# Optimization experiments

Hardware: AMD Instinct MI355X
Metric: run time of the kernel (lower is better)

## Reference

```python
import jax, jax.numpy as jnp
import numpy as np
import math

B, NI, NU, D, H, MAXNB, T = 1024, 50000, 20000, 256, 4, 20, 1000


def _cosine_sqrt_ab():
    t = jnp.linspace(0.0, T, T + 1) / T
    ab = jnp.cos((t + 0.008) / 1.008 * math.pi / 2) ** 2
    ab = ab / ab[0]
    ab = ab[1:]
    return jnp.sqrt(ab), jnp.sqrt(1.0 - ab)


def _ln(x, g, b, eps=1e-5):
    m = jnp.mean(x, -1, keepdims=True)
    v = jnp.var(x, -1, keepdims=True)
    return (x - m) / jnp.sqrt(v + eps) * g + b


def _mha(q, k, v, wqkv, bqkv, wo, bo):
    # torch nn.MultiheadAttention (batch_first) with packed in_proj
    d = q.shape[-1]
    dh = d // H
    wq, wk, wv = jnp.split(wqkv, 3, axis=0)
    bq, bk, bv = jnp.split(bqkv, 3, axis=0)
    def heads(x, w, bb):
        y = x @ w.T + bb
        return y.reshape(x.shape[0], x.shape[1], H, dh).transpose(0, 2, 1, 3)
    qh, kh, vh = heads(q, wq, bq), heads(k, wk, bk), heads(v, wv, bv)
    att = jax.nn.softmax(jnp.einsum('bhqd,bhkd->bhqk', qh, kh) / math.sqrt(dh), axis=-1)
    o = jnp.einsum('bhqk,bhkd->bhqd', att, vh)
    o = o.transpose(0, 2, 1, 3).reshape(q.shape[0], q.shape[1], d)
    return o @ wo.T + bo


def setup_inputs() -> dict:
    key = jax.random.key(0)
    ks = iter(jax.random.split(key, 64))
    p = lambda shape, s=0.02: jax.random.normal(next(ks), shape, jnp.float32) * s
    inp = {}
    inp['x0'] = (jax.random.uniform(next(ks), (B, NI)) < 0.05).astype(jnp.float32)
    inp['user_ids'] = jax.random.randint(next(ks), (B,), 0, NU)
    inp['t'] = jax.random.randint(next(ks), (B,), 0, T)
    inp['noise'] = jax.random.normal(next(ks), (B, D), jnp.float32)
    inp['neighbor_idx'] = jax.random.randint(next(ks), (NU, MAXNB), 0, NI)
    inp['item_emb'] = p((NI, D), 0.01)
    inp['enc_w1'] = p((2 * D, NI), 0.01); inp['enc_b1'] = jnp.zeros((2 * D,))
    inp['enc_w2'] = p((D, 2 * D)); inp['enc_b2'] = jnp.zeros((D,))
    inp['dec_w1'] = p((2 * D, D)); inp['dec_b1'] = jnp.zeros((2 * D,))
    inp['dec_w2'] = p((NI, 2 * D)); inp['dec_b2'] = jnp.zeros((NI,))
    inp['up_w'] = p((D, D)); inp['up_b'] = jnp.zeros((D,))
    inp['ip_w'] = p((D, D)); inp['ip_b'] = jnp.zeros((D,))
    inp['te_w1'] = p((32, 1)); inp['te_b1'] = jnp.zeros((32,))
    inp['te_w2'] = p((D, 32)); inp['te_b2'] = jnp.zeros((D,))
    inp['ca_wqkv'] = p((3 * D, D)); inp['ca_bqkv'] = jnp.zeros((3 * D,))
    inp['ca_wo'] = p((D, D)); inp['ca_bo'] = jnp.zeros((D,))
    inp['sa_wqkv'] = p((3 * D, D)); inp['sa_bqkv'] = jnp.zeros((3 * D,))
    inp['sa_wo'] = p((D, D)); inp['sa_bo'] = jnp.zeros((D,))
    inp['n1_g'] = jnp.ones((D,)); inp['n1_b'] = jnp.zeros((D,))
    inp['n2_g'] = jnp.ones((D,)); inp['n2_b'] = jnp.zeros((D,))
    inp['ff_w1'] = p((2 * D, D)); inp['ff_b1'] = jnp.zeros((2 * D,))
    inp['ff_w2'] = p((D, 2 * D)); inp['ff_b2'] = jnp.zeros((D,))
    return inp


def reference(x0, user_ids, t, noise, neighbor_idx, item_emb,
              enc_w1, enc_b1, enc_w2, enc_b2, dec_w1, dec_b1, dec_w2, dec_b2,
              up_w, up_b, ip_w, ip_b, te_w1, te_b1, te_w2, te_b2,
              ca_wqkv, ca_bqkv, ca_wo, ca_bo, sa_wqkv, sa_bqkv, sa_wo, sa_bo,
              n1_g, n1_b, n2_g, n2_b, ff_w1, ff_b1, ff_w2, ff_b2):
    gelu = lambda x: jax.nn.gelu(x, approximate=False)
    # encoder: (B, NI) -> (B, D)
    z0 = gelu(x0 @ enc_w1.T + enc_b1) @ enc_w2.T + enc_b2
    sqrt_ab, sqrt_1ab = _cosine_sqrt_ab()
    z_t = sqrt_ab[t][:, None] * z0 + sqrt_1ab[t][:, None] * noise
    # vectorized padded neighbor gather: (B, MAXNB, D)
    nb = item_emb[neighbor_idx[user_ids]]
    t_norm = t.astype(jnp.float32) / T
    # denoiser
    q = (z_t @ up_w.T + up_b)[:, None, :]
    kv = nb @ ip_w.T + ip_b
    te = jax.nn.silu(t_norm[:, None] @ te_w1.T + te_b1) @ te_w2.T + te_b2
    q = q + te[:, None, :]
    ca = _mha(q, kv, kv, ca_wqkv, ca_bqkv, ca_wo, ca_bo)
    h = _ln(q + ca, n1_g, n1_b)[:, 0, :]
    sa = _mha(h[:, None], h[:, None], h[:, None], sa_wqkv, sa_bqkv, sa_wo, sa_bo)[:, 0, :]
    h = _ln(h + sa, n2_g, n2_b)
    z_pred = h + (gelu(h @ ff_w1.T + ff_b1) @ ff_w2.T + ff_b2)
    diff_loss = jnp.mean((z_pred - z0) ** 2)
    logits = gelu(z0 @ dec_w1.T + dec_b1) @ dec_w2.T + dec_b2
    recon = jnp.mean(jax.nn.softplus(logits) - logits * x0)
    return diff_loss + 0.1 * recon
```

## Files before the change

kernel.cpp:

```cpp
#include <hip/hip_runtime.h>
#include <math.h>

#define NI   50000
#define Tt   1000
#define KP   50176
#define MW   1568
#define NPAD 50048

typedef __bf16 bf16x8 __attribute__((ext_vector_type(8)));
typedef float  f32x4  __attribute__((ext_vector_type(4)));

__device__ __forceinline__ unsigned short f2bf(float f) {
  unsigned u = __float_as_uint(f);
  u += 0x7FFFu + ((u >> 16) & 1u);
  return (unsigned short)(u >> 16);
}
__device__ __forceinline__ float bf2f(unsigned short u) {
  return __uint_as_float(((unsigned)u) << 16);
}
__device__ __forceinline__ unsigned pack2(float a, float b) {
  return (unsigned)f2bf(a) | ((unsigned)f2bf(b) << 16);
}
__device__ __forceinline__ f32x4 mfma16(const unsigned short* a, const unsigned short* b, f32x4 c) {
  typedef unsigned short u16x8 __attribute__((ext_vector_type(8)));
  u16x8 av = *(const u16x8*)a;
  u16x8 bv = *(const u16x8*)b;
  return __builtin_amdgcn_mfma_f32_16x16x32_bf16(
      __builtin_bit_cast(bf16x8, av), __builtin_bit_cast(bf16x8, bv), c, 0, 0, 0);
}
__device__ __forceinline__ float gelu_f(float x) {
  return 0.5f * x * (1.f + erff(x * 0.70710678118654752f));
}

#define GLD16(gsrc, ldst) __builtin_amdgcn_global_load_lds( \
    (const __attribute__((address_space(1))) unsigned int*)(const void*)(gsrc), \
    (__attribute__((address_space(3))) unsigned int*)(void*)(ldst), 16, 0, 0)

__global__ __launch_bounds__(256) void bm_expand(
    const float* __restrict__ x0, unsigned int* __restrict__ xmask,
    unsigned short* __restrict__ x0b)
{
  __shared__ unsigned int nib[256];
  int r = blockIdx.y, tid = threadIdx.x;
  int c0 = blockIdx.x * 2048;
  int k = c0 + tid * 8;
  const float* row = x0 + (size_t)r * NI;
  float4 a = make_float4(0.f, 0.f, 0.f, 0.f), b = a;
  if (k + 8 <= NI) {
    a = *(const float4*)(row + k);
    b = *(const float4*)(row + k + 4);
  }
  uint4 o;
  o.x = (a.x != 0.f ? 0x3F80u : 0u) | (a.y != 0.f ? 0x3F800000u : 0u);
  o.y = (a.z != 0.f ? 0x3F80u : 0u) | (a.w != 0.f ? 0x3F800000u : 0u);
  o.z = (b.x != 0.f ? 0x3F80u : 0u) | (b.y != 0.f ? 0x3F800000u : 0u);
  o.w = (b.z != 0.f ? 0x3F80u : 0u) | (b.w != 0.f ? 0x3F800000u : 0u);
  if (k < KP) *(uint4*)(x0b + (size_t)r * KP + k) = o;
  unsigned bits8 =
      (a.x != 0.f ? 1u : 0u)  | (a.y != 0.f ? 2u : 0u)  |
      (a.z != 0.f ? 4u : 0u)  | (a.w != 0.f ? 8u : 0u)  |
      (b.x != 0.f ? 16u : 0u) | (b.y != 0.f ? 32u : 0u) |
      (b.z != 0.f ? 64u : 0u) | (b.w != 0.f ? 128u : 0u);
  nib[tid] = bits8;
  __syncthreads();
  if (tid < 64) {
    unsigned wv = nib[tid * 4] | (nib[tid * 4 + 1] << 8) |
                  (nib[tid * 4 + 2] << 16) | (nib[tid * 4 + 3] << 24);
    int widx = (c0 >> 5) + tid;
    if (widx < MW) xmask[(size_t)r * MW + widx] = wv;
  }
}

__global__ __launch_bounds__(256) void cvt_w1(const float* __restrict__ src,
                                              unsigned short* __restrict__ dst) {
  int c = blockIdx.x * 2048 + threadIdx.x * 8;
  if (c >= KP) return;
  int r = blockIdx.y;
  const float* s = src + (size_t)r * NI;
  uint4 o;
  if (c + 8 <= NI) {
    float4 a = *(const float4*)(s + c), b = *(const float4*)(s + c + 4);
    o.x = pack2(a.x, a.y); o.y = pack2(a.z, a.w);
    o.z = pack2(b.x, b.y); o.w = pack2(b.z, b.w);
  } else {
    float v[8];
#pragma unroll
    for (int i = 0; i < 8; ++i) v[i] = (c + i < NI) ? s[c + i] : 0.f;
    o.x = pack2(v[0], v[1]); o.y = pack2(v[2], v[3]);
    o.z = pack2(v[4], v[5]); o.w = pack2(v[6], v[7]);
  }
  *(uint4*)(dst + (size_t)r * KP + c) = o;
}

__global__ __launch_bounds__(256) void cvt_w2n(const float* __restrict__ src,
                                               unsigned short* __restrict__ dst) {
  size_t idx = ((size_t)blockIdx.x * 256 + threadIdx.x) * 8;
  float4 a = *(const float4*)(src + idx), b = *(const float4*)(src + idx + 4);
  uint4 o;
  o.x = pack2(a.x, a.y); o.y = pack2(a.z, a.w);
  o.z = pack2(b.x, b.y); o.w = pack2(b.z, b.w);
  *(uint4*)(dst + idx) = o;
}

__global__ __launch_bounds__(256) void cvt_many(
    const float* s0, const float* s1, const float* s2, const float* s3,
    const float* s4, const float* s5, const float* s6,
    unsigned short* d0, unsigned short* d1, unsigned short* d2, unsigned short* d3,
    unsigned short* d4, unsigned short* d5, unsigned short* d6)
{
  const float* srcs[7] = {s0, s1, s2, s3, s4, s5, s6};
  unsigned short* dsts[7] = {d0, d1, d2, d3, d4, d5, d6};
  const int ns[7] = {131072, 65536, 65536, 65536, 131072, 131072, 131072};
  int j = blockIdx.y;
  int i = (blockIdx.x * 256 + threadIdx.x) * 8;
  if (i >= ns[j]) return;
  float4 a = *(const float4*)(srcs[j] + i), b = *(const float4*)(srcs[j] + i + 4);
  uint4 o;
  o.x = pack2(a.x, a.y); o.y = pack2(a.z, a.w);
  o.z = pack2(b.x, b.y); o.w = pack2(b.z, b.w);
  *(uint4*)(dsts[j] + i) = o;
}

__global__ __launch_bounds__(256) void compose_k(
    const float* __restrict__ ca_wqkv, const float* __restrict__ ca_bqkv,
    const float* __restrict__ ip_w, const float* __restrict__ ip_b,
    const float* __restrict__ sa_wqkv, const float* __restrict__ sa_bqkv,
    const float* __restrict__ sa_wo, const float* __restrict__ sa_bo,
    unsigned short* __restrict__ Wkv, float* __restrict__ bkv,
    unsigned short* __restrict__ Wsa, float* __restrict__ bsa)
{
  int b = blockIdx.x, k = threadIdx.x;
  if (b < 512) {
    const float* wrow = ca_wqkv + (size_t)(256 + b) * 256;
    float s = 0.f;
    for (int c = 0; c < 256; ++c) s += wrow[c] * ip_w[c * 256 + k];
    Wkv[b * 256 + k] = f2bf(s);
    if (k == 0) {
      float sb = 0.f;
      for (int c = 0; c < 256; ++c) sb += wrow[c] * ip_b[c];
      bkv[b] = sb + ca_bqkv[256 + b];
    }
  } else {
    int i = b - 512;
    const float* worow = sa_wo + (size_t)i * 256;
    float s = 0.f;
    for (int c = 0; c < 256; ++c) s += worow[c] * sa_wqkv[(512 + c) * 256 + k];
    Wsa[i * 256 + k] = f2bf(s);
    if (k == 0) {
      float sb = 0.f;
      for (int c = 0; c < 256; ++c) sb += worow[c] * sa_bqkv[512 + c];
      bsa[i] = sb + sa_bo[i];
    }
  }
}

template<int T>
__global__ __launch_bounds__(256) void gemm128(
    const unsigned short* __restrict__ A, int lda,
    const unsigned short* __restrict__ Bw, int ldb,
    const float* __restrict__ bias, void* __restrict__ Cv, int ldc, int K,
    const unsigned int* __restrict__ xmask, float* __restrict__ loss, int Nvalid)
{
  __shared__ __align__(16) unsigned short As[128 * 32];
  __shared__ __align__(16) unsigned short Bs[128 * 32];
  __shared__ unsigned int msk[128][4];
  __shared__ float red[4];
  const int tid = threadIdx.x;
  int m0, n0, kb = 0, kc = 0, iters;
  if (T == 2) {
    int id = blockIdx.x;
    int g = (id & 7) + 8 * (id >> 6);
    m0 = ((id >> 3) & 7) * 128;
    n0 = (g & 3) * 128;
    kc = g >> 2;
    kb = kc * 1568;
    iters = 49;
  } else if (T == 1) {
    int id = blockIdx.x;
    int n = (id & 7) + 8 * (id >> 6);
    if (n >= 391) return;
    m0 = ((id >> 3) & 7) * 128;
    n0 = n * 128;
    iters = 16;
  } else {
    m0 = blockIdx.x * 128; n0 = blockIdx.y * 128;
    iters = K >> 5;
  }
  const int w = tid >> 6, l = tid & 63;
  const int wm = (w >> 1) * 64, wn = (w & 1) * 64;
  const int fr = l & 15, fo = (l >> 4) * 8;
  const int s0 = tid, s1 = tid + 256;
  f32x4 acc[4][4] = {};
  for (int it = 0; it < iters; ++it) {
    int k0 = kb + it * 32;
    __syncthreads();
    GLD16(A  + (size_t)(m0 + (s0 >> 2)) * lda + k0 + (s0 & 3) * 8, &As[s0 * 8]);
    GLD16(A  + (size_t)(m0 + (s1 >> 2)) * lda + k0 + (s1 & 3) * 8, &As[s1 * 8]);
    GLD16(Bw + (size_t)(n0 + (s0 >> 2)) * ldb + k0 + (s0 & 3) * 8, &Bs[s0 * 8]);
    GLD16(Bw + (size_t)(n0 + (s1 >> 2)) * ldb + k0 + (s1 & 3) * 8, &Bs[s1 * 8]);
    __syncthreads();
    const unsigned short *ap[4], *bp[4];
#pragma unroll
    for (int i = 0; i < 4; ++i) {
      ap[i] = &As[(wm + 16 * i + fr) * 32 + fo];
      bp[i] = &Bs[(wn + 16 * i + fr) * 32 + fo];
    }
#pragma unroll
    for (int i = 0; i < 4; ++i)
#pragma unroll
      for (int j = 0; j < 4; ++j)
        acc[i][j] = mfma16(ap[i], bp[j], acc[i][j]);
  }
  const int cr = (l >> 4) * 4, cc = l & 15;
  if (T == 0) {
    unsigned short* Cb = (unsigned short*)Cv;
#pragma unroll
    for (int j = 0; j < 4; ++j) {
      int n = n0 + wn + 16 * j + cc;
      float bv = bias[n];
#pragma unroll
      for (int i = 0; i < 4; ++i)
#pragma unroll
        for (int r = 0; r < 4; ++r) {
          int m = m0 + wm + 16 * i + cr + r;
          Cb[(size_t)m * ldc + n] = f2bf(acc[i][j][r] + bv);
        }
    }
  } else if (T == 2) {
    float* Cp = ((kc < 16) ? (float*)Cv : loss) + (size_t)(kc & 15) * 524288;
#pragma unroll
    for (int i = 0; i < 4; ++i)
#pragma unroll
      for (int j = 0; j < 4; ++j) {
        int n = n0 + wn + 16 * j + cc;
#pragma unroll
        for (int r = 0; r < 4; ++r) {
          int m = m0 + wm + 16 * i + cr + r;
          Cp[(size_t)m * 512 + n] = acc[i][j][r];
        }
      }
  } else {
    {
      int row = tid >> 1, p = tid & 1;
      *(uint2*)&msk[row][p * 2] =
          *(const uint2*)(xmask + (size_t)(m0 + row) * MW + (n0 >> 5) + p * 2);
    }
    __syncthreads();
    float ts = 0.f;
#pragma unroll
    for (int j = 0; j < 4; ++j) {
      int nl = wn + 16 * j + cc;
      int n = n0 + nl;
      if (n < Nvalid) {
        float bv = bias[n];
#pragma unroll
        for (int i = 0; i < 4; ++i)
#pragma unroll
          for (int r = 0; r < 4; ++r) {
            int ml = wm + 16 * i + cr + r;
            float lg = acc[i][j][r] + bv;
            float sp = fmaxf(lg, 0.f) + __logf(1.f + __expf(-fabsf(lg)));
            unsigned word = msk[ml][nl >> 5];
            ts += sp - (((word >> (nl & 31)) & 1u) ? lg : 0.f);
          }
      }
    }
    for (int off = 32; off > 0; off >>= 1) ts += __shfl_xor(ts, off);
    if (l == 0) red[w] = ts;
    __syncthreads();
    if (tid == 0) atomicAdd(loss, red[0] + red[1] + red[2] + red[3]);
  }
}

template<int EPI>
__global__ __launch_bounds__(256) void gemm64(
    const unsigned short* __restrict__ A, int lda,
    const unsigned short* __restrict__ Bw, int ldb,
    const float* __restrict__ bias, void* __restrict__ Cv, int ldc, int K,
    const void* __restrict__ R0, const void* __restrict__ R1, const void* __restrict__ R2,
    void* __restrict__ W0, void* __restrict__ W1, float* __restrict__ loss)
{
  __shared__ __align__(16) unsigned short As[64 * 32];
  __shared__ __align__(16) unsigned short Bs[64 * 32];
  __shared__ float red[4];
  const int tid = threadIdx.x;
  const int m0 = blockIdx.x * 64, n0 = blockIdx.y * 64;
  const int w = tid >> 6, l = tid & 63;
  const int wm = (w >> 1) * 32, wn = (w & 1) * 32;
  const int fr = l & 15, fo = (l >> 4) * 8;
  const int srow = tid >> 2, scol = (tid & 3) * 8;
  f32x4 acc[2][2] = {};
  for (int k0 = 0; k0 < K; k0 += 32) {
    __syncthreads();
    GLD16(A  + (size_t)(m0 + srow) * lda + k0 + scol, &As[tid * 8]);
    GLD16(Bw + (size_t)(n0 + srow) * ldb + k0 + scol, &Bs[tid * 8]);
    __syncthreads();
    const unsigned short* ap0 = &As[(wm +      fr) * 32 + fo];
    const unsigned short* ap1 = &As[(wm + 16 + fr) * 32 + fo];
    const unsigned short* bp0 = &Bs[(wn +      fr) * 32 + fo];
    const unsigned short* bp1 = &Bs[(wn + 16 + fr) * 32 + fo];
    acc[0][0] = mfma16(ap0, bp0, acc[0][0]);
    acc[0][1] = mfma16(ap0, bp1, acc[0][1]);
    acc[1][0] = mfma16(ap1, bp0, acc[1][0]);
    acc[1][1] = mfma16(ap1, bp1, acc[1][1]);
  }
  const int cr = (l >> 4) * 4, cc = l & 15;
  float ts = 0.f;
#pragma unroll
  for (int i = 0; i < 2; ++i)
#pragma unroll
    for (int j = 0; j < 2; ++j) {
      int n = n0 + wn + 16 * j + cc;
      float bv = bias[n];
#pragma unroll
      for (int r = 0; r < 4; ++r) {
        int m = m0 + wm + 16 * i + cr + r;
        float v = acc[i][j][r] + bv;
        size_t idx = (size_t)m * ldc + n;
        if (EPI == 0) ((float*)Cv)[idx] = v;
        if (EPI == 1) ((unsigned short*)Cv)[idx] = f2bf(v);
        if (EPI == 2) ((unsigned short*)Cv)[idx] = f2bf(gelu_f(v));
        if (EPI == 3) {
          ((float*)Cv)[idx] = v;
          ((unsigned short*)W0)[idx] = f2bf(v);
          float zt = ((const float*)R1)[m] * v +
                     ((const float*)R2)[m] * ((const float*)R0)[idx];
          ((unsigned short*)W1)[idx] = f2bf(zt);
        }
        if (EPI == 4) {
          v += ((const float*)R0)[idx];
          ((unsigned short*)Cv)[idx] = f2bf(v);
        }
        if (EPI == 5) {
          v += bf2f(((const unsigned short*)R0)[idx]);
          float d = v - ((const float*)R1)[idx];
          ts += d * d;
        }
      }
    }
  if (EPI == 5) {
    for (int off = 32; off > 0; off >>= 1) ts += __shfl_xor(ts, off);
    if (l == 0) red[w] = ts;
    __syncthreads();
    if (tid == 0) atomicAdd(loss, red[0] + red[1] + red[2] + red[3]);
  }
}

__global__ __launch_bounds__(256) void h1_epi(const float* __restrict__ P0,
                                              const float* __restrict__ P1,
                                              const float* __restrict__ b,
                                              unsigned short* __restrict__ H) {
  int i = blockIdx.x * 256 + threadIdx.x;
  float s = b[i & 511];
#pragma unroll
  for (int k = 0; k < 16; ++k) s += P0[(size_t)k * 524288 + i];
#pragma unroll
  for (int k = 0; k < 16; ++k) s += P1[(size_t)k * 524288 + i];
  H[i] = f2bf(gelu_f(s));
}

__global__ __launch_bounds__(256) void prep_te(
    const int* __restrict__ t,
    const float* __restrict__ te_w1, const float* __restrict__ te_b1,
    const float* __restrict__ te_w2, const float* __restrict__ te_b2,
    float* __restrict__ te, float* __restrict__ sab, float* __restrict__ s1ab)
{
  __shared__ float sj[32];
  int b = blockIdx.x, d = threadIdx.x;
  int ti = t[b];
  float tn = (float)ti / (float)Tt;
  if (d < 32) {
    float a = tn * te_w1[d] + te_b1[d];
    sj[d] = a / (1.f + __expf(-a));
  }
  if (d == 0) {
    double tt = (double)(ti + 1) / (double)Tt;
    double c  = cos((tt + 0.008) / 1.008 * M_PI * 0.5);
    double c0 = cos((0.008) / 1.008 * M_PI * 0.5);
    double ab = (c * c) / (c0 * c0);
    sab[b]  = (float)sqrt(ab);
    s1ab[b] = (float)sqrt(1.0 - ab);
  }
  __syncthreads();
  float accv = te_b2[d];
#pragma unroll
  for (int j = 0; j < 32; ++j) accv += sj[j] * te_w2[d * 32 + j];
  te[(size_t)b * 256 + d] = accv;
}

__global__ __launch_bounds__(256) void gather_nb(
    const int* __restrict__ uid, const int* __restrict__ nidx,
    const float* __restrict__ emb, unsigned short* __restrict__ nb)
{
  int b = blockIdx.x, j = blockIdx.y, d = threadIdx.x;
  int idx = nidx[uid[b] * 20 + j];
  nb[((size_t)b * 20 + j) * 256 + d] = f2bf(emb[(size_t)idx * 256 + d]);
}

__global__ __launch_bounds__(256) void attn_k(
    const float* __restrict__ qh, const unsigned short* __restrict__ kvh,
    unsigned short* __restrict__ o)
{
  int b = blockIdx.x, tid = threadIdx.x;
  int h = tid >> 6, d = tid & 63;
  float qv = qh[(size_t)b * 256 + h * 64 + d];
  const unsigned short* kbase = kvh + (size_t)b * 20 * 512 + h * 64 + d;
  const unsigned short* vbase = kbase + 256;
  float s[20];
#pragma unroll
  for (int k = 0; k < 20; ++k) {
    float p = qv * bf2f(kbase[k * 512]);
    for (int off = 32; off > 0; off >>= 1) p += __shfl_xor(p, off);
    s[k] = p * 0.125f;
  }
  float mx = s[0];
#pragma unroll
  for (int k = 1; k < 20; ++k) mx = fmaxf(mx, s[k]);
  float sum = 0.f;
#pragma unroll
  for (int k = 0; k < 20; ++k) { s[k] = __expf(s[k] - mx); sum += s[k]; }
  float inv = 1.f / sum;
  float ov = 0.f;
#pragma unroll
  for (int k = 0; k < 20; ++k) ov += s[k] * bf2f(vbase[k * 512]);
  o[(size_t)b * 256 + h * 64 + d] = f2bf(ov * inv);
}

__global__ __launch_bounds__(256) void ln_k(
    const unsigned short* __restrict__ X, const unsigned short* __restrict__ Y,
    const float* __restrict__ g, const float* __restrict__ bb,
    unsigned short* __restrict__ out)
{
  __shared__ float rs[4], rs2[4];
  int b = blockIdx.x, d = threadIdx.x;
  size_t i = (size_t)b * 256 + d;
  float v = bf2f(X[i]) + bf2f(Y[i]);
  float s = v, s2 = v * v;
  for (int off = 32; off > 0; off >>= 1) { s += __shfl_xor(s, off); s2 += __shfl_xor(s2, off); }
  int w = d >> 6, l = d & 63;
  if (l == 0) { rs[w] = s; rs2[w] = s2; }
  __syncthreads();
  s  = rs[0] + rs[1] + rs[2] + rs[3];
  s2 = rs2[0] + rs2[1] + rs2[2] + rs2[3];
  float mean = s * (1.f / 256.f);
  float var  = s2 * (1.f / 256.f) - mean * mean;
  out[i] = f2bf((v - mean) * rsqrtf(var + 1e-5f) * g[d] + bb[d]);
}

__global__ void final_k(const float* __restrict__ scal, float* __restrict__ out) {
  out[0] = scal[0] * (1.f / (1024.f * 256.f)) + 0.1f * scal[1] * (1.f / (1024.f * 50000.f));
}

extern "C" void kernel_launch(void* const* d_in, const int* in_sizes, int n_in,
                              void* d_out, int out_size, void* d_ws, size_t ws_size,
                              hipStream_t stream) {
  const float* x0      = (const float*)d_in[0];
  const int*   uid     = (const int*)  d_in[1];
  const int*   t       = (const int*)  d_in[2];
  const float* noise   = (const float*)d_in[3];
  const int*   nidx    = (const int*)  d_in[4];
  const float* item_emb= (const float*)d_in[5];
  const float* enc_w1  = (const float*)d_in[6];
  const float* enc_b1  = (const float*)d_in[7];
  const float* enc_w2  = (const float*)d_in[8];
  const float* enc_b2  = (const float*)d_in[9];
  const float* dec_w1  = (const float*)d_in[10];
  const float* dec_b1  = (const float*)d_in[11];
  const float* dec_w2  = (const float*)d_in[12];
  const float* dec_b2  = (const float*)d_in[13];
  const float* up_w    = (const float*)d_in[14];
  const float* up_b    = (const float*)d_in[15];
  const float* ip_w    = (const float*)d_in[16];
  const float* ip_b    = (const float*)d_in[17];
  const float* te_w1   = (const float*)d_in[18];
  const float* te_b1   = (const float*)d_in[19];
  const float* te_w2   = (const float*)d_in[20];
  const float* te_b2   = (const float*)d_in[21];
  const float* ca_wqkv = (const float*)d_in[22];
  const float* ca_bqkv = (const float*)d_in[23];
  const float* ca_wo   = (const float*)d_in[24];
  const float* ca_bo   = (const float*)d_in[25];
  const float* sa_wqkv = (const float*)d_in[26];
  const float* sa_bqkv = (const float*)d_in[27];
  const float* sa_wo   = (const float*)d_in[28];
  const float* sa_bo   = (const float*)d_in[29];
  const float* n1_g    = (const float*)d_in[30];
  const float* n1_b    = (const float*)d_in[31];
  const float* n2_g    = (const float*)d_in[32];
  const float* n2_b    = (const float*)d_in[33];
  const float* ff_w1   = (const float*)d_in[34];
  const float* ff_b1   = (const float*)d_in[35];
  const float* ff_w2   = (const float*)d_in[36];
  const float* ff_b2   = (const float*)d_in[37];
  (void)in_sizes; (void)n_in; (void)out_size; (void)ws_size;

  float* ws   = (float*)d_ws;
  float* scal = ws;
  float* sab  = ws + 4;
  float* s1ab = sab + 1024;
  float* te   = s1ab + 1024;
  float* qhf  = te + 262144;
  float* z0f  = qhf + 262144;
  float* bkv  = z0f + 262144;
  float* bsa  = bkv + 512;
  unsigned int* xmask = (unsigned int*)(bsa + 256);
  unsigned short* sh  = (unsigned short*)(xmask + 1024 * MW);
  float*          OUTp = (float*)sh;
  unsigned short* nbb  = sh;
  unsigned short* kvhb = nbb + 5242880;
  unsigned short* f1b  = kvhb + 10485760;
  unsigned short* Gb   = f1b + 524288;
  unsigned short* x0b  = Gb + 524288;
  unsigned short* w2n  = x0b;
  unsigned short* w1b  = x0b + (size_t)1024 * KP;
  unsigned short* H1b  = w1b + (size_t)512 * KP;
  unsigned short* z0b  = H1b + 524288;
  unsigned short* ztb  = z0b + 262144;
  unsigned short* qpb  = ztb + 262144;
  unsigned short* ob   = qpb + 262144;
  unsigned short* cab  = ob  + 262144;
  unsigned short* hb   = cab + 262144;
  unsigned short* saob = hb  + 262144;
  unsigned short* h2b  = saob+ 262144;
  unsigned short* enc_w2b = h2b + 262144;
  unsigned short* up_wb   = enc_w2b + 131072;
  unsigned short* ca_wqb  = up_wb + 65536;
  unsigned short* ca_wob  = ca_wqb + 65536;
  unsigned short* ff_w1b  = ca_wob + 65536;
  unsigned short* ff_w2b  = ff_w1b + 131072;
  unsigned short* dec_w1b = ff_w2b + 131072;
  unsigned short* Wkv     = dec_w1b + 131072;
  unsigned short* Wsab    = Wkv + 131072;
  float*          OUTp2   = (float*)(Wsab + 131072);

  hipMemsetAsync(scal, 0, 4 * sizeof(float), stream);

  prep_te<<<1024, 256, 0, stream>>>(t, te_w1, te_b1, te_w2, te_b2, te, sab, s1ab);
  bm_expand<<<dim3(25, 1024), 256, 0, stream>>>(x0, xmask, x0b);
  cvt_w1<<<dim3(25, 512), 256, 0, stream>>>(enc_w1, w1b);
  cvt_many<<<dim3(64, 7), 256, 0, stream>>>(enc_w2, up_w, ca_wqkv, ca_wo, ff_w1, ff_w2, dec_w1,
                                            enc_w2b, up_wb, ca_wqb, ca_wob, ff_w1b, ff_w2b, dec_w1b);
  compose_k<<<768, 256, 0, stream>>>(ca_wqkv, ca_bqkv, ip_w, ip_b,
                                     sa_wqkv, sa_bqkv, sa_wo, sa_bo,
                                     Wkv, bkv, Wsab, bsa);

  gemm128<2><<<1024, 256, 0, stream>>>(
      x0b, KP, w1b, KP, nullptr, OUTp, 512, 1568, nullptr, OUTp2, 0);
  h1_epi<<<2048, 256, 0, stream>>>(OUTp, OUTp2, enc_b1, H1b);

  cvt_w2n<<<12500, 256, 0, stream>>>(dec_w2, w2n);

  gather_nb<<<dim3(1024, 20), 256, 0, stream>>>(uid, nidx, item_emb, nbb);
  gemm128<0><<<dim3(160, 4), 256, 0, stream>>>(
      nbb, 256, Wkv, 256, bkv, kvhb, 512, 256, nullptr, nullptr, 0);

  gemm64<3><<<dim3(16, 4), 256, 0, stream>>>(
      H1b, 512, enc_w2b, 512, enc_b2, z0f, 256, 512, noise, sab, s1ab, z0b, ztb, nullptr);

  gemm64<4><<<dim3(16, 4), 256, 0, stream>>>(
      ztb, 256, up_wb, 256, up_b, qpb, 256, 256, te, nullptr, nullptr, nullptr, nullptr, nullptr);
  gemm64<0><<<dim3(16, 4), 256, 0, stream>>>(
      qpb, 256, ca_wqb, 256, ca_bqkv, qhf, 256, 256,
      nullptr, nullptr, nullptr, nullptr, nullptr, nullptr);

  attn_k<<<1024, 256, 0, stream>>>(qhf, kvhb, ob);
  gemm64<1><<<dim3(16, 4), 256, 0, stream>>>(
      ob, 256, ca_wob, 256, ca_bo, cab, 256, 256,
      nullptr, nullptr, nullptr, nullptr, nullptr, nullptr);
  ln_k<<<1024, 256, 0, stream>>>(qpb, cab, n1_g, n1_b, hb);

  gemm64<1><<<dim3(16, 4), 256, 0, stream>>>(
      hb, 256, Wsab, 256, bsa, saob, 256, 256,
      nullptr, nullptr, nullptr, nullptr, nullptr, nullptr);
  ln_k<<<1024, 256, 0, stream>>>(hb, saob, n2_g, n2_b, h2b);

  gemm64<2><<<dim3(16, 8), 256, 0, stream>>>(
      h2b, 256, ff_w1b, 256, ff_b1, f1b, 512, 256,
      nullptr, nullptr, nullptr, nullptr, nullptr, nullptr);
  gemm64<5><<<dim3(16, 4), 256, 0, stream>>>(
      f1b, 512, ff_w2b, 512, ff_b2, nullptr, 256, 512,
      h2b, z0f, nullptr, nullptr, nullptr, &scal[0]);

  gemm64<2><<<dim3(16, 8), 256, 0, stream>>>(
      z0b, 256, dec_w1b, 256, dec_b1, Gb, 512, 256,
      nullptr, nullptr, nullptr, nullptr, nullptr, nullptr);
  gemm128<1><<<3136, 256, 0, stream>>>(
      Gb, 512, w2n, 512, dec_b2, nullptr, 0, 512, xmask, &scal[1], NI);

  final_k<<<1, 1, 0, stream>>>(scal, (float*)d_out);
}
```

Measured before the change: 919.3 us.

## Double-buffer LDS tiles in gemm128 and gemm64 with explicit waitcnt pipelining

```diff
diff --git a/kernel.cpp b/kernel.cpp
--- a/kernel.cpp
+++ b/kernel.cpp
@@ -35,6 +35,9 @@
 #define GLD16(gsrc, ldst) __builtin_amdgcn_global_load_lds( \
     (const __attribute__((address_space(1))) unsigned int*)(const void*)(gsrc), \
     (__attribute__((address_space(3))) unsigned int*)(void*)(ldst), 16, 0, 0)
+
+#define PIPE_FENCE() __builtin_amdgcn_sched_barrier(0)
+#define RAW_BAR()    __builtin_amdgcn_s_barrier()
 
 __global__ __launch_bounds__(256) void bm_expand(
     const float* __restrict__ x0, unsigned int* __restrict__ xmask,
@@ -161,8 +164,8 @@
     const float* __restrict__ bias, void* __restrict__ Cv, int ldc, int K,
     const unsigned int* __restrict__ xmask, float* __restrict__ loss, int Nvalid)
 {
-  __shared__ __align__(16) unsigned short As[128 * 32];
-  __shared__ __align__(16) unsigned short Bs[128 * 32];
+  __shared__ __align__(16) unsigned short As[2][128 * 32];
+  __shared__ __align__(16) unsigned short Bs[2][128 * 32];
   __shared__ unsigned int msk[128][4];
   __shared__ float red[4];
   const int tid = threadIdx.x;
@@ -190,27 +193,49 @@
   const int wm = (w >> 1) * 64, wn = (w & 1) * 64;
   const int fr = l & 15, fo = (l >> 4) * 8;
   const int s0 = tid, s1 = tid + 256;
+  const unsigned short* Ar0 = A  + (size_t)(m0 + (s0 >> 2)) * lda + (s0 & 3) * 8;
+  const unsigned short* Ar1 = A  + (size_t)(m0 + (s1 >> 2)) * lda + (s1 & 3) * 8;
+  const unsigned short* Br0 = Bw + (size_t)(n0 + (s0 >> 2)) * ldb + (s0 & 3) * 8;
+  const unsigned short* Br1 = Bw + (size_t)(n0 + (s1 >> 2)) * ldb + (s1 & 3) * 8;
   f32x4 acc[4][4] = {};
-  for (int it = 0; it < iters; ++it) {
-    int k0 = kb + it * 32;
-    __syncthreads();
-    GLD16(A  + (size_t)(m0 + (s0 >> 2)) * lda + k0 + (s0 & 3) * 8, &As[s0 * 8]);
-    GLD16(A  + (size_t)(m0 + (s1 >> 2)) * lda + k0 + (s1 & 3) * 8, &As[s1 * 8]);
-    GLD16(Bw + (size_t)(n0 + (s0 >> 2)) * ldb + k0 + (s0 & 3) * 8, &Bs[s0 * 8]);
-    GLD16(Bw + (size_t)(n0 + (s1 >> 2)) * ldb + k0 + (s1 & 3) * 8, &Bs[s1 * 8]);
-    __syncthreads();
-    const unsigned short *ap[4], *bp[4];
-#pragma unroll
-    for (int i = 0; i < 4; ++i) {
-      ap[i] = &As[(wm + 16 * i + fr) * 32 + fo];
-      bp[i] = &Bs[(wn + 16 * i + fr) * 32 + fo];
-    }
-#pragma unroll
-    for (int i = 0; i < 4; ++i)
-#pragma unroll
-      for (int j = 0; j < 4; ++j)
-        acc[i][j] = mfma16(ap[i], bp[j], acc[i][j]);
-  }
+
+#define STG128(IT, BUF) do { int kk_ = kb + (IT) * 32;        \
+    GLD16(Ar0 + kk_, &As[BUF][s0 * 8]);                        \
+    GLD16(Ar1 + kk_, &As[BUF][s1 * 8]);                        \
+    GLD16(Br0 + kk_, &Bs[BUF][s0 * 8]);                        \
+    GLD16(Br1 + kk_, &Bs[BUF][s1 * 8]); } while (0)
+
+#define CMP128(BUF) do {                                       \
+    const unsigned short *ap_[4], *bp_[4];                     \
+    _Pragma("unroll") for (int i_ = 0; i_ < 4; ++i_) {         \
+      ap_[i_] = &As[BUF][(wm + 16 * i_ + fr) * 32 + fo];       \
+      bp_[i_] = &Bs[BUF][(wn + 16 * i_ + fr) * 32 + fo]; }     \
+    _Pragma("unroll") for (int i_ = 0; i_ < 4; ++i_)           \
+    _Pragma("unroll") for (int j_ = 0; j_ < 4; ++j_)           \
+      acc[i_][j_] = mfma16(ap_[i_], bp_[j_], acc[i_][j_]); } while (0)
+
+  STG128(0, 0);
+  STG128(1, 1);
+  for (int it = 0; it < iters; it += 2) {
+    if (it + 1 < iters) asm volatile("s_waitcnt vmcnt(4)" ::: "memory");
+    else                asm volatile("s_waitcnt vmcnt(0)" ::: "memory");
+    PIPE_FENCE(); RAW_BAR(); PIPE_FENCE();
+    CMP128(0);
+    asm volatile("s_waitcnt lgkmcnt(0)" ::: "memory");
+    PIPE_FENCE(); RAW_BAR(); PIPE_FENCE();
+    if (it + 2 < iters) STG128(it + 2, 0);
+    if (it + 1 >= iters) break;
+    if (it + 2 < iters) asm volatile("s_waitcnt vmcnt(4)" ::: "memory");
+    else                asm volatile("s_waitcnt vmcnt(0)" ::: "memory");
+    PIPE_FENCE(); RAW_BAR(); PIPE_FENCE();
+    CMP128(1);
+    asm volatile("s_waitcnt lgkmcnt(0)" ::: "memory");
+    PIPE_FENCE(); RAW_BAR(); PIPE_FENCE();
+    if (it + 3 < iters) STG128(it + 3, 1);
+  }
+#undef STG128
+#undef CMP128
+
   const int cr = (l >> 4) * 4, cc = l & 15;
   if (T == 0) {
     unsigned short* Cb = (unsigned short*)Cv;
@@ -280,8 +305,8 @@
     const void* __restrict__ R0, const void* __restrict__ R1, const void* __restrict__ R2,
     void* __restrict__ W0, void* __restrict__ W1, float* __restrict__ loss)
 {
-  __shared__ __align__(16) unsigned short As[64 * 32];
-  __shared__ __align__(16) unsigned short Bs[64 * 32];
+  __shared__ __align__(16) unsigned short As[2][64 * 32];
+  __shared__ __align__(16) unsigned short Bs[2][64 * 32];
   __shared__ float red[4];
   const int tid = threadIdx.x;
   const int m0 = blockIdx.x * 64, n0 = blockIdx.y * 64;
@@ -289,21 +314,47 @@
   const int wm = (w >> 1) * 32, wn = (w & 1) * 32;
   const int fr = l & 15, fo = (l >> 4) * 8;
   const int srow = tid >> 2, scol = (tid & 3) * 8;
+  const unsigned short* Ar = A  + (size_t)(m0 + srow) * lda + scol;
+  const unsigned short* Br = Bw + (size_t)(n0 + srow) * ldb + scol;
+  const int iters = K >> 5;
   f32x4 acc[2][2] = {};
-  for (int k0 = 0; k0 < K; k0 += 32) {
-    __syncthreads();
-    GLD16(A  + (size_t)(m0 + srow) * lda + k0 + scol, &As[tid * 8]);
-    GLD16(Bw + (size_t)(n0 + srow) * ldb + k0 + scol, &Bs[tid * 8]);
-    __syncthreads();
-    const unsigned short* ap0 = &As[(wm +      fr) * 32 + fo];
-    const unsigned short* ap1 = &As[(wm + 16 + fr) * 32 + fo];
-    const unsigned short* bp0 = &Bs[(wn +      fr) * 32 + fo];
-    const unsigned short* bp1 = &Bs[(wn + 16 + fr) * 32 + fo];
-    acc[0][0] = mfma16(ap0, bp0, acc[0][0]);
-    acc[0][1] = mfma16(ap0, bp1, acc[0][1]);
-    acc[1][0] = mfma16(ap1, bp0, acc[1][0]);
-    acc[1][1] = mfma16(ap1, bp1, acc[1][1]);
-  }
+
+#define STG64(IT, BUF) do { int kk_ = (IT) * 32;               \
+    GLD16(Ar + kk_, &As[BUF][tid * 8]);                        \
+    GLD16(Br + kk_, &Bs[BUF][tid * 8]); } while (0)
+
+#define CMP64(BUF) do {                                        \
+    const unsigned short* a0_ = &As[BUF][(wm +      fr) * 32 + fo]; \
+    const unsigned short* a1_ = &As[BUF][(wm + 16 + fr) * 32 + fo]; \
+    const unsigned short* b0_ = &Bs[BUF][(wn +      fr) * 32 + fo]; \
+    const unsigned short* b1_ = &Bs[BUF][(wn + 16 + fr) * 32 + fo]; \
+    acc[0][0] = mfma16(a0_, b0_, acc[0][0]);                   \
+    acc[0][1] = mfma16(a0_, b1_, acc[0][1]);                   \
+    acc[1][0] = mfma16(a1_, b0_, acc[1][0]);                   \
+    acc[1][1] = mfma16(a1_, b1_, acc[1][1]); } while (0)
+
+  STG64(0, 0);
+  STG64(1, 1);
+  for (int it = 0; it < iters; it += 2) {
+    if (it + 1 < iters) asm volatile("s_waitcnt vmcnt(2)" ::: "memory");
+    else                asm volatile("s_waitcnt vmcnt(0)" ::: "memory");
+    PIPE_FENCE(); RAW_BAR(); PIPE_FENCE();
+    CMP64(0);
+    asm volatile("s_waitcnt lgkmcnt(0)" ::: "memory");
+    PIPE_FENCE(); RAW_BAR(); PIPE_FENCE();
+    if (it + 2 < iters) STG64(it + 2, 0);
+    if (it + 1 >= iters) break;
+    if (it + 2 < iters) asm volatile("s_waitcnt vmcnt(2)" ::: "memory");
+    else                asm volatile("s_waitcnt vmcnt(0)" ::: "memory");
+    PIPE_FENCE(); RAW_BAR(); PIPE_FENCE();
+    CMP64(1);
+    asm volatile("s_waitcnt lgkmcnt(0)" ::: "memory");
+    PIPE_FENCE(); RAW_BAR(); PIPE_FENCE();
+    if (it + 3 < iters) STG64(it + 3, 1);
+  }
+#undef STG64
+#undef CMP64
+
   const int cr = (l >> 4) * 4, cc = l & 15;
   float ts = 0.f;
 #pragma unroll
```

Result: no change. 911.0 us (-0.9%).

## Expand bitmask into bf16 A tiles inside encoder GEMM with double-buffered B

Applied to the files above, without the earlier changes.

```diff
diff --git a/kernel.cpp b/kernel.cpp
--- a/kernel.cpp
+++ b/kernel.cpp
@@ -36,9 +36,11 @@
     (const __attribute__((address_space(1))) unsigned int*)(const void*)(gsrc), \
     (__attribute__((address_space(3))) unsigned int*)(void*)(ldst), 16, 0, 0)
 
+#define PIPE_FENCE() __builtin_amdgcn_sched_barrier(0)
+#define RAW_BAR()    __builtin_amdgcn_s_barrier()
+
 __global__ __launch_bounds__(256) void bm_expand(
-    const float* __restrict__ x0, unsigned int* __restrict__ xmask,
-    unsigned short* __restrict__ x0b)
+    const float* __restrict__ x0, unsigned int* __restrict__ xmask)
 {
   __shared__ unsigned int nib[256];
   int r = blockIdx.y, tid = threadIdx.x;
@@ -50,12 +52,6 @@
     a = *(const float4*)(row + k);
     b = *(const float4*)(row + k + 4);
   }
-  uint4 o;
-  o.x = (a.x != 0.f ? 0x3F80u : 0u) | (a.y != 0.f ? 0x3F800000u : 0u);
-  o.y = (a.z != 0.f ? 0x3F80u : 0u) | (a.w != 0.f ? 0x3F800000u : 0u);
-  o.z = (b.x != 0.f ? 0x3F80u : 0u) | (b.y != 0.f ? 0x3F800000u : 0u);
-  o.w = (b.z != 0.f ? 0x3F80u : 0u) | (b.w != 0.f ? 0x3F800000u : 0u);
-  if (k < KP) *(uint4*)(x0b + (size_t)r * KP + k) = o;
   unsigned bits8 =
       (a.x != 0.f ? 1u : 0u)  | (a.y != 0.f ? 2u : 0u)  |
       (a.z != 0.f ? 4u : 0u)  | (a.w != 0.f ? 8u : 0u)  |
@@ -154,6 +150,97 @@
   }
 }
 
+__global__ __launch_bounds__(256) void enc_gemm(
+    const unsigned int* __restrict__ xmask,
+    const unsigned short* __restrict__ Bw,
+    float* __restrict__ P0, float* __restrict__ P1)
+{
+  __shared__ __align__(16) unsigned short As[128 * 32];
+  __shared__ __align__(16) unsigned short Bs[2][128 * 32];
+  const int tid = threadIdx.x;
+  const int id = blockIdx.x;
+  const int g = (id & 7) + 8 * (id >> 6);
+  const int m0 = ((id >> 3) & 7) * 128;
+  const int n0 = (g & 3) * 128;
+  const int kc = g >> 2;
+  const int kb = kc * 1568;
+  const int w = tid >> 6, l = tid & 63;
+  const int wm = (w >> 1) * 64, wn = (w & 1) * 64;
+  const int fr = l & 15, fo = (l >> 4) * 8;
+  const int s0 = tid, s1 = tid + 256;
+  const unsigned short* Br0 = Bw + (size_t)(n0 + (s0 >> 2)) * KP + kb + (s0 & 3) * 8;
+  const unsigned short* Br1 = Bw + (size_t)(n0 + (s1 >> 2)) * KP + kb + (s1 & 3) * 8;
+  const int arow = tid >> 1, ahalf = tid & 1;
+  const unsigned int* mrowp = xmask + (size_t)(m0 + arow) * MW + (kb >> 5);
+  f32x4 acc[4][4] = {};
+
+#define EXPANDA(VW) do {                                                     \
+    unsigned bits_ = ((VW) >> (ahalf * 16)) & 0xFFFFu;                       \
+    uint4 q0_, q1_;                                                          \
+    q0_.x = (bits_ & 1u     ? 0x3F80u : 0u) | (bits_ & 2u     ? 0x3F800000u : 0u); \
+    q0_.y = (bits_ & 4u     ? 0x3F80u : 0u) | (bits_ & 8u     ? 0x3F800000u : 0u); \
+    q0_.z = (bits_ & 16u    ? 0x3F80u : 0u) | (bits_ & 32u    ? 0x3F800000u : 0u); \
+    q0_.w = (bits_ & 64u    ? 0x3F80u : 0u) | (bits_ & 128u   ? 0x3F800000u : 0u); \
+    q1_.x = (bits_ & 256u   ? 0x3F80u : 0u) | (bits_ & 512u   ? 0x3F800000u : 0u); \
+    q1_.y = (bits_ & 1024u  ? 0x3F80u : 0u) | (bits_ & 2048u  ? 0x3F800000u : 0u); \
+    q1_.z = (bits_ & 4096u  ? 0x3F80u : 0u) | (bits_ & 8192u  ? 0x3F800000u : 0u); \
+    q1_.w = (bits_ & 16384u ? 0x3F80u : 0u) | (bits_ & 32768u ? 0x3F800000u : 0u); \
+    *(uint4*)&As[arow * 32 + ahalf * 16]     = q0_;                          \
+    *(uint4*)&As[arow * 32 + ahalf * 16 + 8] = q1_;                          \
+  } while (0)
+
+#define CMPE(BUF) do {                                                       \
+    const unsigned short *ap_[4], *bp_[4];                                   \
+    _Pragma("unroll") for (int i_ = 0; i_ < 4; ++i_) {                       \
+      ap_[i_] = &As[(wm + 16 * i_ + fr) * 32 + fo];                          \
+      bp_[i_] = &Bs[BUF][(wn + 16 * i_ + fr) * 32 + fo]; }                   \
+    _Pragma("unroll") for (int i_ = 0; i_ < 4; ++i_)                         \
+    _Pragma("unroll") for (int j_ = 0; j_ < 4; ++j_)                         \
+      acc[i_][j_] = mfma16(ap_[i_], bp_[j_], acc[i_][j_]); } while (0)
+
+  {
+    unsigned vm = mrowp[0];
+    GLD16(Br0,      &Bs[0][s0 * 8]);
+    GLD16(Br1,      &Bs[0][s1 * 8]);
+    GLD16(Br0 + 32, &Bs[1][s0 * 8]);
+    GLD16(Br1 + 32, &Bs[1][s1 * 8]);
+    EXPANDA(vm);
+    asm volatile("s_waitcnt vmcnt(2) lgkmcnt(0)" ::: "memory");
+    PIPE_FENCE(); RAW_BAR(); PIPE_FENCE();
+  }
+  for (int it = 0; it < 49; ++it) {
+    unsigned vnext = 0;
+    if (it < 48) vnext = mrowp[it + 1];
+    CMPE(it & 1);
+    if (it == 48) break;
+    PIPE_FENCE(); RAW_BAR(); PIPE_FENCE();
+    if (it < 47) {
+      GLD16(Br0 + (it + 2) * 32, &Bs[it & 1][s0 * 8]);
+      GLD16(Br1 + (it + 2) * 32, &Bs[it & 1][s1 * 8]);
+    }
+    EXPANDA(vnext);
+    if (it < 47) asm volatile("s_waitcnt vmcnt(2) lgkmcnt(0)" ::: "memory");
+    else         asm volatile("s_waitcnt vmcnt(0) lgkmcnt(0)" ::: "memory");
+    PIPE_FENCE(); RAW_BAR(); PIPE_FENCE();
+  }
+#undef EXPANDA
+#undef CMPE
+
+  const int cr = (l >> 4) * 4, cc = l & 15;
+  float* Cp = ((kc < 16) ? P0 : P1) + (size_t)(kc & 15) * 524288;
+#pragma unroll
+  for (int i = 0; i < 4; ++i)
+#pragma unroll
+    for (int j = 0; j < 4; ++j) {
+      int n = n0 + wn + 16 * j + cc;
+#pragma unroll
+      for (int r = 0; r < 4; ++r) {
+        int m = m0 + wm + 16 * i + cr + r;
+        Cp[(size_t)m * 512 + n] = acc[i][j][r];
+      }
+    }
+}
+
 template<int T>
 __global__ __launch_bounds__(256) void gemm128(
     const unsigned short* __restrict__ A, int lda,
@@ -166,16 +253,8 @@
   __shared__ unsigned int msk[128][4];
   __shared__ float red[4];
   const int tid = threadIdx.x;
-  int m0, n0, kb = 0, kc = 0, iters;
-  if (T == 2) {
-    int id = blockIdx.x;
-    int g = (id & 7) + 8 * (id >> 6);
-    m0 = ((id >> 3) & 7) * 128;
-    n0 = (g & 3) * 128;
-    kc = g >> 2;
-    kb = kc * 1568;
-    iters = 49;
-  } else if (T == 1) {
+  int m0, n0, iters;
+  if (T == 1) {
     int id = blockIdx.x;
     int n = (id & 7) + 8 * (id >> 6);
     if (n >= 391) return;
@@ -192,7 +271,7 @@
   const int s0 = tid, s1 = tid + 256;
   f32x4 acc[4][4] = {};
   for (int it = 0; it < iters; ++it) {
-    int k0 = kb + it * 32;
+    int k0 = it * 32;
     __syncthreads();
     GLD16(A  + (size_t)(m0 + (s0 >> 2)) * lda + k0 + (s0 & 3) * 8, &As[s0 * 8]);
     GLD16(A  + (size_t)(m0 + (s1 >> 2)) * lda + k0 + (s1 & 3) * 8, &As[s1 * 8]);
@@ -226,19 +305,6 @@
           Cb[(size_t)m * ldc + n] = f2bf(acc[i][j][r] + bv);
         }
     }
-  } else if (T == 2) {
-    float* Cp = ((kc < 16) ? (float*)Cv : loss) + (size_t)(kc & 15) * 524288;
-#pragma unroll
-    for (int i = 0; i < 4; ++i)
-#pragma unroll
-      for (int j = 0; j < 4; ++j) {
-        int n = n0 + wn + 16 * j + cc;
-#pragma unroll
-        for (int r = 0; r < 4; ++r) {
-          int m = m0 + wm + 16 * i + cr + r;
-          Cp[(size_t)m * 512 + n] = acc[i][j][r];
-        }
-      }
   } else {
     {
       int row = tid >> 1, p = tid & 1;
@@ -536,7 +602,7 @@
   hipMemsetAsync(scal, 0, 4 * sizeof(float), stream);
 
   prep_te<<<1024, 256, 0, stream>>>(t, te_w1, te_b1, te_w2, te_b2, te, sab, s1ab);
-  bm_expand<<<dim3(25, 1024), 256, 0, stream>>>(x0, xmask, x0b);
+  bm_expand<<<dim3(25, 1024), 256, 0, stream>>>(x0, xmask);
   cvt_w1<<<dim3(25, 512), 256, 0, stream>>>(enc_w1, w1b);
   cvt_many<<<dim3(64, 7), 256, 0, stream>>>(enc_w2, up_w, ca_wqkv, ca_wo, ff_w1, ff_w2, dec_w1,
                                             enc_w2b, up_wb, ca_wqb, ca_wob, ff_w1b, ff_w2b, dec_w1b);
@@ -544,8 +610,7 @@
                                      sa_wqkv, sa_bqkv, sa_wo, sa_bo,
                                      Wkv, bkv, Wsab, bsa);
 
-  gemm128<2><<<1024, 256, 0, stream>>>(
-      x0b, KP, w1b, KP, nullptr, OUTp, 512, 1568, nullptr, OUTp2, 0);
+  enc_gemm<<<1024, 256, 0, stream>>>(xmask, w1b, OUTp, OUTp2);
   h1_epi<<<2048, 256, 0, stream>>>(OUTp, OUTp2, enc_b1, H1b);
 
   cvt_w2n<<<12500, 256, 0, stream>>>(dec_w2, w2n);
```

Result: faster. 877.7 us (-4.5%).
